# Kernel optimization log

Measured on AMD Instinct MI355X. Metric: run time of the kernel, lower is better.

The kernel has to match this reference:

```python
import jax, jax.numpy as jnp
import numpy as np

B, N, K = 8, 2048, 16
C_IN, C_MID, C_OUT = 64, 16, 64
WH = [32, 32]
FH = [256]


def _mlp_params(key, dims, scale_keyed=True):
    ps = []
    for i in range(len(dims) - 1):
        key, k1 = jax.random.split(key)
        w = jax.random.normal(k1, (dims[i], dims[i + 1]), jnp.float32) / np.sqrt(dims[i])
        b = jnp.zeros((dims[i + 1],), jnp.float32)
        ps += [w, b]
    return ps


def setup_inputs() -> dict:
    key = jax.random.key(0)
    k1, k2, k3, k4, k5 = jax.random.split(key, 5)
    groups = jnp.broadcast_to(jnp.arange(N, dtype=jnp.int32) // K, (B, N))
    points = jax.random.normal(k1, (B, N, 3), jnp.float32)
    feats = jax.random.normal(k2, (B, N, C_IN), jnp.float32)
    point_mask = (jax.random.uniform(k3, (B, N)) > 0.1).astype(jnp.float32)
    w1, b1, w2, b2, w3, b3 = _mlp_params(k4, [3] + WH + [C_MID])
    f1, fb1, f2, fb2 = _mlp_params(k5, [C_IN * C_MID] + FH + [C_OUT])
    return {"groups": groups, "points": points, "feats": feats,
            "point_mask": point_mask,
            "w1": w1, "b1": b1, "w2": w2, "b2": b2, "w3": w3, "b3": b3,
            "f1": f1, "fb1": fb1, "f2": f2, "fb2": fb2}


def _neighbor_idxs(groups):
    # matches[b,i,j] = groups[b,i]==groups[b,j]; torch .nonzero yields, per (b,i),
    # the matching j in increasing order -> stable argsort of ~matches, take first K.
    matches = groups[:, :, None] == groups[:, None, :]            # [B,N,N]
    return jnp.argsort((~matches).astype(jnp.int32), axis=-1)[:, :, :K]  # [B,N,K]


def reference(groups, points, feats, point_mask,
              w1, b1, w2, b2, w3, b3, f1, fb1, f2, fb2):
    idxs = _neighbor_idxs(groups)                                  # [B,N,K] int
    gather = jax.vmap(lambda arr, ix: arr[ix])                     # per-batch gather
    nb_pts = gather(points, idxs)                                  # [B,N,K,3]
    nb_feats = gather(feats, idxs)                                 # [B,N,K,C_IN]
    rel = points[:, :, None, :] - nb_pts                           # [B,N,K,3] (xy encoding = identity)

    # weight_conv: pointwise MLP 3 -> 32 -> 32 -> C_MID, then explicit ReLU
    h = jax.nn.relu(rel @ w1 + b1)
    h = jax.nn.relu(h @ w2 + b2)
    m = jax.nn.relu(h @ w3 + b3)                                   # [B,N,K,C_MID]

    tmask = gather(point_mask, idxs)                               # [B,N,K]
    m = m * tmask[..., None]
    nb_feats = nb_feats * tmask[..., None]

    # per-(point) matmul: [C_MID,K] x [K,C_IN] -> flatten C_MID-major
    e = jnp.einsum('bnkm,bnkc->bnmc', m, nb_feats)                 # [B,N,C_MID,C_IN]
    e = e.reshape(B, N, C_MID * C_IN)

    # final_conv: pointwise MLP 1024 -> 256 -> C_OUT
    h2 = jax.nn.relu(e @ f1 + fb1)
    out = h2 @ f2 + fb2                                            # [B,N,C_OUT]
    return out
```

## Files before the change

kernel.cpp:

```cpp
#include <hip/hip_runtime.h>

typedef unsigned short u16;
typedef short bf16x8 __attribute__((ext_vector_type(8)));
typedef float f32x4  __attribute__((ext_vector_type(4)));
typedef u16   u16x4  __attribute__((ext_vector_type(4)));

__device__ __forceinline__ u16 f2bf(float f) {
  union { float f; unsigned int i; } v; v.f = f;
  unsigned int r = (v.i + 0x7FFFu + ((v.i >> 16) & 1u)) >> 16;
  return (u16)r;
}

__global__ __launch_bounds__(256) void repack_k(const float* __restrict__ f1,
                                                const float* __restrict__ f2,
                                                u16* __restrict__ f1p,
                                                u16* __restrict__ f2p) {
  const int o = blockIdx.x * 256 + threadIdx.x;
  if (o < 262144) {
    const int j = o & 7, n = (o >> 3) & 255, kb = o >> 11;
    f1p[o] = f2bf(f1[(kb * 8 + j) * 256 + n]);
  }
  if (o < 16384) {
    const int j = o & 7, n = (o >> 3) & 63, kb = o >> 9;
    f2p[o] = f2bf(f2[(kb * 8 + j) * 64 + n]);
  }
}

__global__ __launch_bounds__(256, 4) void mlp_einsum_k(
    const float* __restrict__ points, const float* __restrict__ feats,
    const float* __restrict__ pmask,
    const float* __restrict__ w1, const float* __restrict__ b1,
    const float* __restrict__ w2, const float* __restrict__ b2,
    const float* __restrict__ w3, const float* __restrict__ b3,
    const float* __restrict__ f1, const float* __restrict__ f2,
    u16* __restrict__ f1p, u16* __restrict__ f2p,
    u16* __restrict__ Eg) {
  const int gi = blockIdx.x;
  const int bb = blockIdx.y;
  const int base = gi * 16;
  const int t = threadIdx.x;

  __shared__ float Pl[16][3];
  __shared__ float Mask[16];
  __shared__ float F[1024];
  __shared__ float Ml[16 * 16 * 20];

  {
    const int o = (bb * 128 + gi) * 256 + t;
    { const int j = o & 7, n = (o >> 3) & 255, kb = o >> 11;
      f1p[o] = f2bf(f1[(kb * 8 + j) * 256 + n]); }
    if (o < 16384) {
      const int j = o & 7, n = (o >> 3) & 63, kb = o >> 9;
      f2p[o] = f2bf(f2[(kb * 8 + j) * 64 + n]);
    }
  }

  if (t < 16) {
    Mask[t] = pmask[bb * 2048 + base + t];
    const int p = (bb * 2048 + base + t) * 3;
    Pl[t][0] = points[p + 0];
    Pl[t][1] = points[p + 1];
    Pl[t][2] = points[p + 2];
  }
  __syncthreads();

  {
    const int k = t >> 4;
    const float mk = Mask[k];
    const f32x4 fv =
        *(const f32x4*)&feats[(size_t)(bb * 2048 + base) * 64 + t * 4];
    f32x4 fs = { fv.x * mk, fv.y * mk, fv.z * mk, fv.w * mk };
    *(f32x4*)&F[t * 4] = fs;
  }
  {
    const int i = t >> 4, k = t & 15;
    const float r0 = Pl[i][0] - Pl[k][0];
    const float r1 = Pl[i][1] - Pl[k][1];
    const float r2 = Pl[i][2] - Pl[k][2];
    float h1[32];
#pragma unroll
    for (int o = 0; o < 32; ++o) {
      float a = b1[o];
      a = fmaf(r0, w1[o], a);
      a = fmaf(r1, w1[32 + o], a);
      a = fmaf(r2, w1[64 + o], a);
      h1[o] = fmaxf(a, 0.f);
    }
    float h2[32];
#pragma unroll
    for (int o = 0; o < 32; ++o) h2[o] = b2[o];
#pragma unroll
    for (int j = 0; j < 32; ++j) {
      const float hj = h1[j];
      const float* w = &w2[j * 32];
#pragma unroll
      for (int o = 0; o < 32; ++o) h2[o] = fmaf(hj, w[o], h2[o]);
    }
#pragma unroll
    for (int o = 0; o < 32; ++o) h2[o] = fmaxf(h2[o], 0.f);
    float mo[16];
#pragma unroll
    for (int o = 0; o < 16; ++o) mo[o] = b3[o];
#pragma unroll
    for (int j = 0; j < 32; ++j) {
      const float hj = h2[j];
      const float* w = &w3[j * 16];
#pragma unroll
      for (int o = 0; o < 16; ++o) mo[o] = fmaf(hj, w[o], mo[o]);
    }
    const float mk = Mask[k];
    float* Mrow = &Ml[(i * 16 + k) * 20];
#pragma unroll
    for (int o = 0; o < 16; ++o) Mrow[o] = fmaxf(mo[o], 0.f) * mk;
  }
  __syncthreads();

  {
    const int i = t >> 4;
    const int c0 = (t & 15) * 4;
    float acc[16][4] = {};
#pragma unroll
    for (int k = 0; k < 16; ++k) {
      const float* Fr = &F[k * 64 + c0];
      const float f0 = Fr[0], fA = Fr[1], fB = Fr[2], fC = Fr[3];
      const float* Mrow = &Ml[(i * 16 + k) * 20];
#pragma unroll
      for (int mi = 0; mi < 16; ++mi) {
        const float mv = Mrow[mi];
        acc[mi][0] = fmaf(mv, f0, acc[mi][0]);
        acc[mi][1] = fmaf(mv, fA, acc[mi][1]);
        acc[mi][2] = fmaf(mv, fB, acc[mi][2]);
        acc[mi][3] = fmaf(mv, fC, acc[mi][3]);
      }
    }
    u16* Erow = Eg + (size_t)(bb * 2048 + base + i) * 1024;
#pragma unroll
    for (int mi = 0; mi < 16; ++mi) {
      u16x4 v = { f2bf(acc[mi][0]), f2bf(acc[mi][1]),
                  f2bf(acc[mi][2]), f2bf(acc[mi][3]) };
      *(u16x4*)&Erow[mi * 64 + c0] = v;
    }
  }
}

#define STAGE(bf_, kc_)                                                        \
  do {                                                                         \
    const int rl_ = lane >> 3;                                       \
    const int sg_ = (lane & 7) ^ rl_;         \
    const u16* s0_ =                                                           \
        Eg + (size_t)(R + wv * 8 + rl_) * 1024 + (kc_) + sg_ * 8;              \
    u16* d0_ = &Asw[bf_][(wv * 8) * 64];            \
    u16* d1_ = &Asw[bf_][(32 + wv * 8) * 64];                                  \
    __builtin_amdgcn_global_load_lds(                                          \
        (const __attribute__((address_space(1))) void*)s0_,                    \
        (__attribute__((address_space(3))) void*)d0_, 16, 0, 0);               \
    __builtin_amdgcn_global_load_lds(                                          \
        (const __attribute__((address_space(1))) void*)(s0_ + 32 * 1024),      \
        (__attribute__((address_space(3))) void*)d1_, 16, 0, 0);               \
  } while (0)

__global__ __launch_bounds__(256) void gemm_k(
    const u16* __restrict__ Eg, const u16* __restrict__ f1p,
    const float* __restrict__ fb1, const u16* __restrict__ f2p,
    const float* __restrict__ fb2, float* __restrict__ out) {
  const int R = blockIdx.x * 64;
  const int t = threadIdx.x;
  const int wv = t >> 6, lane = t & 63;
  const int q = lane >> 4, r16 = lane & 15;

  __shared__ __align__(16) u16 Asw[3][64 * 64];
  __shared__ __align__(16) u16 H2[64 * 264];

  const int nb = wv * 64;
  f32x4 acc[4][4] = {};

  STAGE(0, 0);
  STAGE(1, 64);
  int cur = 0, stg = 2;
  for (int c = 0; c < 16; ++c) {
    if (c < 15) asm volatile("s_waitcnt vmcnt(2)" ::: "memory");
    else        asm volatile("s_waitcnt vmcnt(0)" ::: "memory");
    __builtin_amdgcn_s_barrier();

    bf16x8 bv[2][4];
#pragma unroll
    for (int ksl = 0; ksl < 2; ++ksl) {
      const int kb = c * 8 + ksl * 4 + q;
#pragma unroll
      for (int nt = 0; nt < 4; ++nt)
        bv[ksl][nt] =
            *(const bf16x8*)&f1p[(size_t)(kb * 256 + nb + nt * 16 + r16) * 8];
    }
    bf16x8 a[2][4];
#pragma unroll
    for (int ksl = 0; ksl < 2; ++ksl)
#pragma unroll
      for (int rt = 0; rt < 4; ++rt) {
        const int r = rt * 16 + r16;
        const int g = (ksl * 4 + q) ^ (r & 7);
        a[ksl][rt] = *(const bf16x8*)&Asw[cur][r * 64 + g * 8];
      }
    __builtin_amdgcn_sched_barrier(0);
    if (c <= 13) STAGE(stg, (c + 2) * 64);
    __builtin_amdgcn_sched_barrier(0);
#pragma unroll
    for (int ksl = 0; ksl < 2; ++ksl)
#pragma unroll
      for (int nt = 0; nt < 4; ++nt)
#pragma unroll
        for (int rt = 0; rt < 4; ++rt)
          acc[rt][nt] = __builtin_amdgcn_mfma_f32_16x16x32_bf16(
              a[ksl][rt], bv[ksl][nt], acc[rt][nt], 0, 0, 0);
    cur = (cur == 2) ? 0 : cur + 1;
    stg = (stg == 2) ? 0 : stg + 1;
  }

#pragma unroll
  for (int nt = 0; nt < 4; ++nt) {
    const int col = nb + nt * 16 + r16;
    const float bias = fb1[col];
#pragma unroll
    for (int rt = 0; rt < 4; ++rt)
#pragma unroll
      for (int r = 0; r < 4; ++r)
        H2[(rt * 16 + q * 4 + r) * 264 + col] =
            f2bf(fmaxf(acc[rt][nt][r] + bias, 0.f));
  }
  __syncthreads();

  const int n0 = wv * 16;
  const float bias2 = fb2[n0 + r16];
#pragma unroll
  for (int rt = 0; rt < 4; ++rt) {
    f32x4 a2 = {};
#pragma unroll
    for (int ks = 0; ks < 8; ++ks) {
      const bf16x8 av =
          *(const bf16x8*)&H2[(rt * 16 + r16) * 264 + ks * 32 + q * 8];
      const bf16x8 b2v =
          *(const bf16x8*)&f2p[(size_t)((ks * 4 + q) * 64 + n0 + r16) * 8];
      a2 = __builtin_amdgcn_mfma_f32_16x16x32_bf16(av, b2v, a2, 0, 0, 0);
    }
#pragma unroll
    for (int r = 0; r < 4; ++r)
      out[(size_t)(R + rt * 16 + q * 4 + r) * 64 + n0 + r16] = a2[r] + bias2;
  }
}
#undef STAGE

__global__ __launch_bounds__(256) void fused_k(
    const float* __restrict__ points, const float* __restrict__ feats,
    const float* __restrict__ pmask,
    const float* __restrict__ w1, const float* __restrict__ b1,
    const float* __restrict__ w2, const float* __restrict__ b2,
    const float* __restrict__ w3, const float* __restrict__ b3,
    const u16* __restrict__ f1p, const float* __restrict__ fb1,
    const u16* __restrict__ f2p, const float* __restrict__ fb2,
    float* __restrict__ out) {
  const int gi = blockIdx.x;
  const int bb = blockIdx.y;
  const int base = gi * 16;
  const int t = threadIdx.x;

  __shared__ float Wl[1712];
  __shared__ float Pl[16][3];
  __shared__ float Mask[16];
  __shared__ float F[1024];
  __shared__ __align__(16) u16 E[16 * 1032];
  __shared__ __align__(16) union {
    float Ml[16 * 16 * 17];
    u16   H2[16 * 264];
  } U;

  for (int idx = t; idx < 96;   idx += 256) Wl[idx]        = w1[idx];
  for (int idx = t; idx < 32;   idx += 256) Wl[96 + idx]   = b1[idx];
  for (int idx = t; idx < 1024; idx += 256) Wl[128 + idx]  = w2[idx];
  for (int idx = t; idx < 32;   idx += 256) Wl[1152 + idx] = b2[idx];
  for (int idx = t; idx < 512;  idx += 256) Wl[1184 + idx] = w3[idx];
  for (int idx = t; idx < 16;   idx += 256) Wl[1696 + idx] = b3[idx];
  if (t < 16) {
    Mask[t] = pmask[bb * 2048 + base + t];
    const int p = (bb * 2048 + base + t) * 3;
    Pl[t][0] = points[p + 0];
    Pl[t][1] = points[p + 1];
    Pl[t][2] = points[p + 2];
  }
  __syncthreads();

  for (int e = t; e < 1024; e += 256) {
    const int k = e >> 6;
    F[e] = feats[(bb * 2048 + base) * 64 + e] * Mask[k];
  }
  {
    const int i = t >> 4, k = t & 15;
    const float r0 = Pl[i][0] - Pl[k][0];
    const float r1 = Pl[i][1] - Pl[k][1];
    const float r2 = Pl[i][2] - Pl[k][2];
    float h1[32];
#pragma unroll
    for (int o = 0; o < 32; ++o) {
      float a = Wl[96 + o];
      a = fmaf(r0, Wl[o], a);
      a = fmaf(r1, Wl[32 + o], a);
      a = fmaf(r2, Wl[64 + o], a);
      h1[o] = fmaxf(a, 0.f);
    }
    float h2[32];
#pragma unroll
    for (int o = 0; o < 32; ++o) h2[o] = Wl[1152 + o];
#pragma unroll
    for (int j = 0; j < 32; ++j) {
      const float hj = h1[j];
      const float* w = &Wl[128 + j * 32];
#pragma unroll
      for (int o = 0; o < 32; ++o) h2[o] = fmaf(hj, w[o], h2[o]);
    }
#pragma unroll
    for (int o = 0; o < 32; ++o) h2[o] = fmaxf(h2[o], 0.f);
    float mo[16];
#pragma unroll
    for (int o = 0; o < 16; ++o) mo[o] = Wl[1696 + o];
#pragma unroll
    for (int j = 0; j < 32; ++j) {
      const float hj = h2[j];
      const float* w = &Wl[1184 + j * 16];
#pragma unroll
      for (int o = 0; o < 16; ++o) mo[o] = fmaf(hj, w[o], mo[o]);
    }
    const float mk = Mask[k];
    float* Mrow = &U.Ml[(i * 16 + k) * 17];
#pragma unroll
    for (int o = 0; o < 16; ++o) Mrow[o] = fmaxf(mo[o], 0.f) * mk;
  }
  __syncthreads();

  {
    const int i = t >> 4;
    const int c0 = (t & 15) * 4;
    float acc[16][4] = {};
#pragma unroll
    for (int k = 0; k < 16; ++k) {
      const float* Fr = &F[k * 64 + c0];
      const float f0 = Fr[0], fA = Fr[1], fB = Fr[2], fC = Fr[3];
      const float* Mrow = &U.Ml[(i * 16 + k) * 17];
#pragma unroll
      for (int mi = 0; mi < 16; ++mi) {
        const float mv = Mrow[mi];
        acc[mi][0] = fmaf(mv, f0, acc[mi][0]);
        acc[mi][1] = fmaf(mv, fA, acc[mi][1]);
        acc[mi][2] = fmaf(mv, fB, acc[mi][2]);
        acc[mi][3] = fmaf(mv, fC, acc[mi][3]);
      }
    }
    __syncthreads();
#pragma unroll
    for (int mi = 0; mi < 16; ++mi) {
      u16x4 v = { f2bf(acc[mi][0]), f2bf(acc[mi][1]), f2bf(acc[mi][2]), f2bf(acc[mi][3]) };
      *(u16x4*)&E[i * 1032 + mi * 64 + c0] = v;
    }
  }
  __syncthreads();

  {
    const int wv = t >> 6;
    const int lane = t & 63;
    const int q = lane >> 4, r16 = lane & 15;
    const int nb = wv * 64;
    f32x4 acc[4] = {};
    for (int ks = 0; ks < 32; ++ks) {
      const int k0 = ks * 32;
      const bf16x8 a = *(const bf16x8*)&E[r16 * 1032 + k0 + q * 8];
      const int kb = (k0 >> 3) + q;
#pragma unroll
      for (int nt = 0; nt < 4; ++nt) {
        const bf16x8 bvv = *(const bf16x8*)&f1p[(kb * 256 + nb + nt * 16 + r16) * 8];
        acc[nt] = __builtin_amdgcn_mfma_f32_16x16x32_bf16(a, bvv, acc[nt], 0, 0, 0);
      }
    }
    __syncthreads();
#pragma unroll
    for (int nt = 0; nt < 4; ++nt) {
      const int col = nb + nt * 16 + r16;
      const float bias = fb1[col];
#pragma unroll
      for (int r = 0; r < 4; ++r)
        U.H2[(q * 4 + r) * 264 + col] = f2bf(fmaxf(acc[nt][r] + bias, 0.f));
    }
  }
  __syncthreads();

  {
    const int wv = t >> 6;
    const int lane = t & 63;
    const int q = lane >> 4, r16 = lane & 15;
    const int n0 = wv * 16;
    f32x4 acc = {};
#pragma unroll
    for (int ks = 0; ks < 8; ++ks) {
      const int k0 = ks * 32;
      const bf16x8 a = *(const bf16x8*)&U.H2[r16 * 264 + k0 + q * 8];
      const bf16x8 bvv = *(const bf16x8*)&f2p[(((k0 >> 3) + q) * 64 + n0 + r16) * 8];
      acc = __builtin_amdgcn_mfma_f32_16x16x32_bf16(a, bvv, acc, 0, 0, 0);
    }
    const int col = n0 + r16;
    const float bias = fb2[col];
#pragma unroll
    for (int r = 0; r < 4; ++r) {
      const int row = q * 4 + r;
      out[((size_t)(bb * 2048 + base + row)) * 64 + col] = acc[r] + bias;
    }
  }
}

extern "C" void kernel_launch(void* const* d_in, const int* in_sizes, int n_in,
                              void* d_out, int out_size, void* d_ws, size_t ws_size,
                              hipStream_t stream) {
  const float* points = (const float*)d_in[1];
  const float* feats  = (const float*)d_in[2];
  const float* pmask  = (const float*)d_in[3];
  const float* w1 = (const float*)d_in[4];
  const float* b1 = (const float*)d_in[5];
  const float* w2 = (const float*)d_in[6];
  const float* b2 = (const float*)d_in[7];
  const float* w3 = (const float*)d_in[8];
  const float* b3 = (const float*)d_in[9];
  const float* f1 = (const float*)d_in[10];
  const float* fb1 = (const float*)d_in[11];
  const float* f2 = (const float*)d_in[12];
  const float* fb2 = (const float*)d_in[13];
  float* out = (float*)d_out;

  u16* f1p = (u16*)d_ws;
  u16* f2p = f1p + 262144;
  const size_t NEED = 524288 + 32768 + (size_t)16384 * 1024 * 2;

  if (ws_size >= NEED) {
    u16* Eg = f2p + 16384;
    mlp_einsum_k<<<dim3(128, 8), dim3(256), 0, stream>>>(
        points, feats, pmask, w1, b1, w2, b2, w3, b3, f1, f2, f1p, f2p, Eg);
    gemm_k<<<dim3(256), dim3(256), 0, stream>>>(Eg, f1p, fb1, f2p, fb2, out);
  } else {
    repack_k<<<dim3(1024), dim3(256), 0, stream>>>(f1, f2, f1p, f2p);
    fused_k<<<dim3(128, 8), dim3(256), 0, stream>>>(points, feats, pmask,
                                                    w1, b1, w2, b2, w3, b3,
                                                    f1p, fb1, f2p, fb2, out);
  }
}
```

Before: 130.0 us.

## Fuse weight MLP, einsum and final MLP into one 64-row mega kernel

Adds a single kernel with about 150KB of dynamic LDS. Each block computes the E matrix for 64 rows (four groups of 16) in shared memory, then runs both bf16 MFMA GEMMs directly from LDS. This removes the 32MB global round trip of the E intermediate between the two-kernel path. It also moves the f1/f2 bf16 repack back into a separate launch. The trade-off is one block per CU with only 256 blocks, so latency hiding is limited and the four group phases run serially within each block.

```diff
diff --git a/kernel.cpp b/kernel.cpp
--- a/kernel.cpp
+++ b/kernel.cpp
@@ -26,14 +26,187 @@
   }
 }
 
+#define MEGA_LDS 153088
+
+__global__ __launch_bounds__(256, 1) void mega_k(
+    const float* __restrict__ points, const float* __restrict__ feats,
+    const float* __restrict__ pmask,
+    const float* __restrict__ w1, const float* __restrict__ b1,
+    const float* __restrict__ w2, const float* __restrict__ b2,
+    const float* __restrict__ w3, const float* __restrict__ b3,
+    const u16* __restrict__ f1p, const float* __restrict__ fb1,
+    const u16* __restrict__ f2p, const float* __restrict__ fb2,
+    float* __restrict__ out) {
+  extern __shared__ __align__(16) char smem[];
+  u16*   E    = (u16*)smem;
+  u16*   H2   = (u16*)smem;
+  float* Ml   = (float*)(smem + 132096);
+  float* F    = (float*)(smem + 148736);
+  float* Pl   = (float*)(smem + 152832);
+  float* Mask = (float*)(smem + 153024);
+
+  const int t = threadIdx.x;
+  const int wv = t >> 6, lane = t & 63;
+  const int q = lane >> 4, r16 = lane & 15;
+  const int RB = blockIdx.x * 64;
+  const int bb = RB >> 11;
+  const int rowb = bb * 2048;
+
+  for (int g = 0; g < 4; ++g) {
+    const int base = (RB & 2047) + g * 16;
+    if (t < 16) {
+      Mask[t] = pmask[rowb + base + t];
+      const int p = (rowb + base + t) * 3;
+      Pl[t * 3 + 0] = points[p + 0];
+      Pl[t * 3 + 1] = points[p + 1];
+      Pl[t * 3 + 2] = points[p + 2];
+    }
+    __syncthreads();
+
+    {
+      const int k = t >> 4;
+      const float mk = Mask[k];
+      const f32x4 fv =
+          *(const f32x4*)&feats[(size_t)(rowb + base) * 64 + t * 4];
+      f32x4 fs = { fv.x * mk, fv.y * mk, fv.z * mk, fv.w * mk };
+      *(f32x4*)&F[t * 4] = fs;
+    }
+    {
+      const int i = t >> 4, k = t & 15;
+      const float r0 = Pl[i * 3 + 0] - Pl[k * 3 + 0];
+      const float r1 = Pl[i * 3 + 1] - Pl[k * 3 + 1];
+      const float r2 = Pl[i * 3 + 2] - Pl[k * 3 + 2];
+      float h1[32];
+#pragma unroll
+      for (int o = 0; o < 32; ++o) {
+        float a = b1[o];
+        a = fmaf(r0, w1[o], a);
+        a = fmaf(r1, w1[32 + o], a);
+        a = fmaf(r2, w1[64 + o], a);
+        h1[o] = fmaxf(a, 0.f);
+      }
+      float h2[32];
+#pragma unroll
+      for (int o = 0; o < 32; ++o) h2[o] = b2[o];
+#pragma unroll
+      for (int j = 0; j < 32; ++j) {
+        const float hj = h1[j];
+        const float* w = &w2[j * 32];
+#pragma unroll
+        for (int o = 0; o < 32; ++o) h2[o] = fmaf(hj, w[o], h2[o]);
+      }
+#pragma unroll
+      for (int o = 0; o < 32; ++o) h2[o] = fmaxf(h2[o], 0.f);
+      float mo[16];
+#pragma unroll
+      for (int o = 0; o < 16; ++o) mo[o] = b3[o];
+#pragma unroll
+      for (int j = 0; j < 32; ++j) {
+        const float hj = h2[j];
+        const float* w = &w3[j * 16];
+#pragma unroll
+        for (int o = 0; o < 16; ++o) mo[o] = fmaf(hj, w[o], mo[o]);
+      }
+      const float mk = Mask[k];
+      float* Mrow = &Ml[i * 260 + k * 16];
+#pragma unroll
+      for (int o = 0; o < 16; ++o) Mrow[o] = fmaxf(mo[o], 0.f) * mk;
+    }
+    __syncthreads();
+
+    {
+      const int i = t >> 4;
+      const int c0 = (t & 15) * 4;
+      float acc[16][4] = {};
+#pragma unroll
+      for (int k = 0; k < 16; ++k) {
+        const float* Fr = &F[k * 64 + c0];
+        const float f0 = Fr[0], fA = Fr[1], fB = Fr[2], fC = Fr[3];
+        const float* Mv = &Ml[i * 260 + k * 16];
+#pragma unroll
+        for (int mi = 0; mi < 16; ++mi) {
+          const float mv = Mv[mi];
+          acc[mi][0] = fmaf(mv, f0, acc[mi][0]);
+          acc[mi][1] = fmaf(mv, fA, acc[mi][1]);
+          acc[mi][2] = fmaf(mv, fB, acc[mi][2]);
+          acc[mi][3] = fmaf(mv, fC, acc[mi][3]);
+        }
+      }
+      u16* Erow = &E[(g * 16 + i) * 1032];
+#pragma unroll
+      for (int mi = 0; mi < 16; ++mi) {
+        u16x4 v = { f2bf(acc[mi][0]), f2bf(acc[mi][1]),
+                    f2bf(acc[mi][2]), f2bf(acc[mi][3]) };
+        *(u16x4*)&Erow[mi * 64 + c0] = v;
+      }
+    }
+    __syncthreads();
+  }
+
+  const int nb = wv * 64;
+  f32x4 acc[4][4] = {};
+  for (int c = 0; c < 16; ++c) {
+#pragma unroll
+    for (int ksl = 0; ksl < 2; ++ksl) {
+      const int kb = c * 8 + ksl * 4 + q;
+      bf16x8 bvv[4];
+#pragma unroll
+      for (int nt = 0; nt < 4; ++nt)
+        bvv[nt] =
+            *(const bf16x8*)&f1p[(size_t)(kb * 256 + nb + nt * 16 + r16) * 8];
+      bf16x8 av[4];
+#pragma unroll
+      for (int rt = 0; rt < 4; ++rt)
+        av[rt] = *(const bf16x8*)&E[(rt * 16 + r16) * 1032 + c * 64 +
+                                    ksl * 32 + q * 8];
+#pragma unroll
+      for (int nt = 0; nt < 4; ++nt)
+#pragma unroll
+        for (int rt = 0; rt < 4; ++rt)
+          acc[rt][nt] = __builtin_amdgcn_mfma_f32_16x16x32_bf16(
+              av[rt], bvv[nt], acc[rt][nt], 0, 0, 0);
+    }
+  }
+  __syncthreads();
+
+#pragma unroll
+  for (int nt = 0; nt < 4; ++nt) {
+    const int col = nb + nt * 16 + r16;
+    const float bias = fb1[col];
+#pragma unroll
+    for (int rt = 0; rt < 4; ++rt)
+#pragma unroll
+      for (int r = 0; r < 4; ++r)
+        H2[(rt * 16 + q * 4 + r) * 264 + col] =
+            f2bf(fmaxf(acc[rt][nt][r] + bias, 0.f));
+  }
+  __syncthreads();
+
+  const int n0 = wv * 16;
+  const float bias2 = fb2[n0 + r16];
+#pragma unroll
+  for (int rt = 0; rt < 4; ++rt) {
+    f32x4 a2 = {};
+#pragma unroll
+    for (int ks = 0; ks < 8; ++ks) {
+      const bf16x8 av =
+          *(const bf16x8*)&H2[(rt * 16 + r16) * 264 + ks * 32 + q * 8];
+      const bf16x8 b2v =
+          *(const bf16x8*)&f2p[(size_t)((ks * 4 + q) * 64 + n0 + r16) * 8];
+      a2 = __builtin_amdgcn_mfma_f32_16x16x32_bf16(av, b2v, a2, 0, 0, 0);
+    }
+#pragma unroll
+    for (int r = 0; r < 4; ++r)
+      out[(size_t)(RB + rt * 16 + q * 4 + r) * 64 + n0 + r16] = a2[r] + bias2;
+  }
+}
+
 __global__ __launch_bounds__(256, 4) void mlp_einsum_k(
     const float* __restrict__ points, const float* __restrict__ feats,
     const float* __restrict__ pmask,
     const float* __restrict__ w1, const float* __restrict__ b1,
     const float* __restrict__ w2, const float* __restrict__ b2,
     const float* __restrict__ w3, const float* __restrict__ b3,
-    const float* __restrict__ f1, const float* __restrict__ f2,
-    u16* __restrict__ f1p, u16* __restrict__ f2p,
     u16* __restrict__ Eg) {
   const int gi = blockIdx.x;
   const int bb = blockIdx.y;
@@ -43,17 +216,7 @@
   __shared__ float Pl[16][3];
   __shared__ float Mask[16];
   __shared__ float F[1024];
-  __shared__ float Ml[16 * 16 * 20];
-
-  {
-    const int o = (bb * 128 + gi) * 256 + t;
-    { const int j = o & 7, n = (o >> 3) & 255, kb = o >> 11;
-      f1p[o] = f2bf(f1[(kb * 8 + j) * 256 + n]); }
-    if (o < 16384) {
-      const int j = o & 7, n = (o >> 3) & 63, kb = o >> 9;
-      f2p[o] = f2bf(f2[(kb * 8 + j) * 64 + n]);
-    }
-  }
+  __shared__ float Ml[16 * 260];
 
   if (t < 16) {
     Mask[t] = pmask[bb * 2048 + base + t];
@@ -63,7 +226,6 @@
     Pl[t][2] = points[p + 2];
   }
   __syncthreads();
-
   {
     const int k = t >> 4;
     const float mk = Mask[k];
@@ -109,12 +271,11 @@
       for (int o = 0; o < 16; ++o) mo[o] = fmaf(hj, w[o], mo[o]);
     }
     const float mk = Mask[k];
-    float* Mrow = &Ml[(i * 16 + k) * 20];
+    float* Mrow = &Ml[i * 260 + k * 16];
 #pragma unroll
     for (int o = 0; o < 16; ++o) Mrow[o] = fmaxf(mo[o], 0.f) * mk;
   }
   __syncthreads();
-
   {
     const int i = t >> 4;
     const int c0 = (t & 15) * 4;
@@ -123,10 +284,10 @@
     for (int k = 0; k < 16; ++k) {
       const float* Fr = &F[k * 64 + c0];
       const float f0 = Fr[0], fA = Fr[1], fB = Fr[2], fC = Fr[3];
-      const float* Mrow = &Ml[(i * 16 + k) * 20];
+      const float* Mv = &Ml[i * 260 + k * 16];
 #pragma unroll
       for (int mi = 0; mi < 16; ++mi) {
-        const float mv = Mrow[mi];
+        const float mv = Mv[mi];
         acc[mi][0] = fmaf(mv, f0, acc[mi][0]);
         acc[mi][1] = fmaf(mv, fA, acc[mi][1]);
         acc[mi][2] = fmaf(mv, fB, acc[mi][2]);
@@ -145,11 +306,11 @@
 
 #define STAGE(bf_, kc_)                                                        \
   do {                                                                         \
-    const int rl_ = lane >> 3;                                       \
-    const int sg_ = (lane & 7) ^ rl_;         \
+    const int rl_ = lane >> 3;                                                 \
+    const int sg_ = (lane & 7) ^ rl_;                                          \
     const u16* s0_ =                                                           \
         Eg + (size_t)(R + wv * 8 + rl_) * 1024 + (kc_) + sg_ * 8;              \
-    u16* d0_ = &Asw[bf_][(wv * 8) * 64];            \
+    u16* d0_ = &Asw[bf_][(wv * 8) * 64];                                       \
     u16* d1_ = &Asw[bf_][(32 + wv * 8) * 64];                                  \
     __builtin_amdgcn_global_load_lds(                                          \
         (const __attribute__((address_space(1))) void*)s0_,                    \
@@ -247,170 +408,6 @@
   }
 }
 #undef STAGE
-
-__global__ __launch_bounds__(256) void fused_k(
-    const float* __restrict__ points, const float* __restrict__ feats,
-    const float* __restrict__ pmask,
-    const float* __restrict__ w1, const float* __restrict__ b1,
-    const float* __restrict__ w2, const float* __restrict__ b2,
-    const float* __restrict__ w3, const float* __restrict__ b3,
-    const u16* __restrict__ f1p, const float* __restrict__ fb1,
-    const u16* __restrict__ f2p, const float* __restrict__ fb2,
-    float* __restrict__ out) {
-  const int gi = blockIdx.x;
-  const int bb = blockIdx.y;
-  const int base = gi * 16;
-  const int t = threadIdx.x;
-
-  __shared__ float Wl[1712];
-  __shared__ float Pl[16][3];
-  __shared__ float Mask[16];
-  __shared__ float F[1024];
-  __shared__ __align__(16) u16 E[16 * 1032];
-  __shared__ __align__(16) union {
-    float Ml[16 * 16 * 17];
-    u16   H2[16 * 264];
-  } U;
-
-  for (int idx = t; idx < 96;   idx += 256) Wl[idx]        = w1[idx];
-  for (int idx = t; idx < 32;   idx += 256) Wl[96 + idx]   = b1[idx];
-  for (int idx = t; idx < 1024; idx += 256) Wl[128 + idx]  = w2[idx];
-  for (int idx = t; idx < 32;   idx += 256) Wl[1152 + idx] = b2[idx];
-  for (int idx = t; idx < 512;  idx += 256) Wl[1184 + idx] = w3[idx];
-  for (int idx = t; idx < 16;   idx += 256) Wl[1696 + idx] = b3[idx];
-  if (t < 16) {
-    Mask[t] = pmask[bb * 2048 + base + t];
-    const int p = (bb * 2048 + base + t) * 3;
-    Pl[t][0] = points[p + 0];
-    Pl[t][1] = points[p + 1];
-    Pl[t][2] = points[p + 2];
-  }
-  __syncthreads();
-
-  for (int e = t; e < 1024; e += 256) {
-    const int k = e >> 6;
-    F[e] = feats[(bb * 2048 + base) * 64 + e] * Mask[k];
-  }
-  {
-    const int i = t >> 4, k = t & 15;
-    const float r0 = Pl[i][0] - Pl[k][0];
-    const float r1 = Pl[i][1] - Pl[k][1];
-    const float r2 = Pl[i][2] - Pl[k][2];
-    float h1[32];
-#pragma unroll
-    for (int o = 0; o < 32; ++o) {
-      float a = Wl[96 + o];
-      a = fmaf(r0, Wl[o], a);
-      a = fmaf(r1, Wl[32 + o], a);
-      a = fmaf(r2, Wl[64 + o], a);
-      h1[o] = fmaxf(a, 0.f);
-    }
-    float h2[32];
-#pragma unroll
-    for (int o = 0; o < 32; ++o) h2[o] = Wl[1152 + o];
-#pragma unroll
-    for (int j = 0; j < 32; ++j) {
-      const float hj = h1[j];
-      const float* w = &Wl[128 + j * 32];
-#pragma unroll
-      for (int o = 0; o < 32; ++o) h2[o] = fmaf(hj, w[o], h2[o]);
-    }
-#pragma unroll
-    for (int o = 0; o < 32; ++o) h2[o] = fmaxf(h2[o], 0.f);
-    float mo[16];
-#pragma unroll
-    for (int o = 0; o < 16; ++o) mo[o] = Wl[1696 + o];
-#pragma unroll
-    for (int j = 0; j < 32; ++j) {
-      const float hj = h2[j];
-      const float* w = &Wl[1184 + j * 16];
-#pragma unroll
-      for (int o = 0; o < 16; ++o) mo[o] = fmaf(hj, w[o], mo[o]);
-    }
-    const float mk = Mask[k];
-    float* Mrow = &U.Ml[(i * 16 + k) * 17];
-#pragma unroll
-    for (int o = 0; o < 16; ++o) Mrow[o] = fmaxf(mo[o], 0.f) * mk;
-  }
-  __syncthreads();
-
-  {
-    const int i = t >> 4;
-    const int c0 = (t & 15) * 4;
-    float acc[16][4] = {};
-#pragma unroll
-    for (int k = 0; k < 16; ++k) {
-      const float* Fr = &F[k * 64 + c0];
-      const float f0 = Fr[0], fA = Fr[1], fB = Fr[2], fC = Fr[3];
-      const float* Mrow = &U.Ml[(i * 16 + k) * 17];
-#pragma unroll
-      for (int mi = 0; mi < 16; ++mi) {
-        const float mv = Mrow[mi];
-        acc[mi][0] = fmaf(mv, f0, acc[mi][0]);
-        acc[mi][1] = fmaf(mv, fA, acc[mi][1]);
-        acc[mi][2] = fmaf(mv, fB, acc[mi][2]);
-        acc[mi][3] = fmaf(mv, fC, acc[mi][3]);
-      }
-    }
-    __syncthreads();
-#pragma unroll
-    for (int mi = 0; mi < 16; ++mi) {
-      u16x4 v = { f2bf(acc[mi][0]), f2bf(acc[mi][1]), f2bf(acc[mi][2]), f2bf(acc[mi][3]) };
-      *(u16x4*)&E[i * 1032 + mi * 64 + c0] = v;
-    }
-  }
-  __syncthreads();
-
-  {
-    const int wv = t >> 6;
-    const int lane = t & 63;
-    const int q = lane >> 4, r16 = lane & 15;
-    const int nb = wv * 64;
-    f32x4 acc[4] = {};
-    for (int ks = 0; ks < 32; ++ks) {
-      const int k0 = ks * 32;
-      const bf16x8 a = *(const bf16x8*)&E[r16 * 1032 + k0 + q * 8];
-      const int kb = (k0 >> 3) + q;
-#pragma unroll
-      for (int nt = 0; nt < 4; ++nt) {
-        const bf16x8 bvv = *(const bf16x8*)&f1p[(kb * 256 + nb + nt * 16 + r16) * 8];
-        acc[nt] = __builtin_amdgcn_mfma_f32_16x16x32_bf16(a, bvv, acc[nt], 0, 0, 0);
-      }
-    }
-    __syncthreads();
-#pragma unroll
-    for (int nt = 0; nt < 4; ++nt) {
-      const int col = nb + nt * 16 + r16;
-      const float bias = fb1[col];
-#pragma unroll
-      for (int r = 0; r < 4; ++r)
-        U.H2[(q * 4 + r) * 264 + col] = f2bf(fmaxf(acc[nt][r] + bias, 0.f));
-    }
-  }
-  __syncthreads();
-
-  {
-    const int wv = t >> 6;
-    const int lane = t & 63;
-    const int q = lane >> 4, r16 = lane & 15;
-    const int n0 = wv * 16;
-    f32x4 acc = {};
-#pragma unroll
-    for (int ks = 0; ks < 8; ++ks) {
-      const int k0 = ks * 32;
-      const bf16x8 a = *(const bf16x8*)&U.H2[r16 * 264 + k0 + q * 8];
-      const bf16x8 bvv = *(const bf16x8*)&f2p[(((k0 >> 3) + q) * 64 + n0 + r16) * 8];
-      acc = __builtin_amdgcn_mfma_f32_16x16x32_bf16(a, bvv, acc, 0, 0, 0);
-    }
-    const int col = n0 + r16;
-    const float bias = fb2[col];
-#pragma unroll
-    for (int r = 0; r < 4; ++r) {
-      const int row = q * 4 + r;
-      out[((size_t)(bb * 2048 + base + row)) * 64 + col] = acc[r] + bias;
-    }
-  }
-}
 
 extern "C" void kernel_launch(void* const* d_in, const int* in_sizes, int n_in,
                               void* d_out, int out_size, void* d_ws, size_t ws_size,
@@ -432,17 +429,25 @@
 
   u16* f1p = (u16*)d_ws;
   u16* f2p = f1p + 262144;
-  const size_t NEED = 524288 + 32768 + (size_t)16384 * 1024 * 2;
-
-  if (ws_size >= NEED) {
+
+  static int mega_ok = -1;
+  if (mega_ok < 0) {
+    hipError_t e = hipFuncSetAttribute(
+        reinterpret_cast<const void*>(mega_k),
+        hipFuncAttributeMaxDynamicSharedMemorySize, MEGA_LDS);
+    mega_ok = (e == hipSuccess) ? 1 : 0;
+  }
+
+  if (mega_ok && ws_size >= 524288 + 32768) {
+    repack_k<<<dim3(1024), dim3(256), 0, stream>>>(f1, f2, f1p, f2p);
+    mega_k<<<dim3(256), dim3(256), MEGA_LDS, stream>>>(
+        points, feats, pmask, w1, b1, w2, b2, w3, b3,
+        f1p, fb1, f2p, fb2, out);
+  } else {
     u16* Eg = f2p + 16384;
+    repack_k<<<dim3(1024), dim3(256), 0, stream>>>(f1, f2, f1p, f2p);
     mlp_einsum_k<<<dim3(128, 8), dim3(256), 0, stream>>>(
-        points, feats, pmask, w1, b1, w2, b2, w3, b3, f1, f2, f1p, f2p, Eg);
+        points, feats, pmask, w1, b1, w2, b2, w3, b3, Eg);
     gemm_k<<<dim3(256), dim3(256), 0, stream>>>(Eg, f1p, fb1, f2p, fb2, out);
-  } else {
-    repack_k<<<dim3(1024), dim3(256), 0, stream>>>(f1, f2, f1p, f2p);
-    fused_k<<<dim3(128, 8), dim3(256), 0, stream>>>(points, feats, pmask,
-                                                    w1, b1, w2, b2, w3, b3,
-                                                    f1p, fb1, f2p, fb2, out);
-  }
-}
+  }
+}
```

Measured after the change: 169.8 us. 1.31x slower.

## Split GEMM work across eight waves and halve einsum accumulator registers

Applied to the files above, without the earlier changes.

The GEMM kernel now launches 512 threads per block: eight waves in a 2x4 grid, each computing 32 rows by 64 columns instead of 64x64. Each wave issues one LDS staging load per chunk instead of two, and the vmcnt wait is adjusted to match. In the einsum kernel, the 16x4 accumulator is computed in two halves of 8 to cut register pressure, and the Ml layout changes from a padded stride of 20 to a per-point stride of 260. The goal is more waves in flight on the GEMM and better occupancy in the einsum. The cost is that every wave in the GEMM reloads its f1p B fragments, so B traffic per block doubles.

```diff
diff --git a/kernel.cpp b/kernel.cpp
--- a/kernel.cpp
+++ b/kernel.cpp
@@ -43,7 +43,7 @@
   __shared__ float Pl[16][3];
   __shared__ float Mask[16];
   __shared__ float F[1024];
-  __shared__ float Ml[16 * 16 * 20];
+  __shared__ float Ml[16 * 260];
 
   {
     const int o = (bb * 128 + gi) * 256 + t;
@@ -109,7 +109,7 @@
       for (int o = 0; o < 16; ++o) mo[o] = fmaf(hj, w[o], mo[o]);
     }
     const float mk = Mask[k];
-    float* Mrow = &Ml[(i * 16 + k) * 20];
+    float* Mrow = &Ml[i * 260 + k * 16];
 #pragma unroll
     for (int o = 0; o < 16; ++o) Mrow[o] = fmaxf(mo[o], 0.f) * mk;
   }
@@ -118,67 +118,67 @@
   {
     const int i = t >> 4;
     const int c0 = (t & 15) * 4;
-    float acc[16][4] = {};
-#pragma unroll
-    for (int k = 0; k < 16; ++k) {
-      const float* Fr = &F[k * 64 + c0];
-      const float f0 = Fr[0], fA = Fr[1], fB = Fr[2], fC = Fr[3];
-      const float* Mrow = &Ml[(i * 16 + k) * 20];
-#pragma unroll
-      for (int mi = 0; mi < 16; ++mi) {
-        const float mv = Mrow[mi];
-        acc[mi][0] = fmaf(mv, f0, acc[mi][0]);
-        acc[mi][1] = fmaf(mv, fA, acc[mi][1]);
-        acc[mi][2] = fmaf(mv, fB, acc[mi][2]);
-        acc[mi][3] = fmaf(mv, fC, acc[mi][3]);
+    u16* Erow = Eg + (size_t)(bb * 2048 + base + i) * 1024;
+#pragma unroll
+    for (int half = 0; half < 2; ++half) {
+      float acc[8][4] = {};
+#pragma unroll
+      for (int k = 0; k < 16; ++k) {
+        const float* Fr = &F[k * 64 + c0];
+        const float f0 = Fr[0], fA = Fr[1], fB = Fr[2], fC = Fr[3];
+        const float* Mv = &Ml[i * 260 + k * 16 + half * 8];
+#pragma unroll
+        for (int mi = 0; mi < 8; ++mi) {
+          const float mv = Mv[mi];
+          acc[mi][0] = fmaf(mv, f0, acc[mi][0]);
+          acc[mi][1] = fmaf(mv, fA, acc[mi][1]);
+          acc[mi][2] = fmaf(mv, fB, acc[mi][2]);
+          acc[mi][3] = fmaf(mv, fC, acc[mi][3]);
+        }
       }
-    }
-    u16* Erow = Eg + (size_t)(bb * 2048 + base + i) * 1024;
-#pragma unroll
-    for (int mi = 0; mi < 16; ++mi) {
-      u16x4 v = { f2bf(acc[mi][0]), f2bf(acc[mi][1]),
-                  f2bf(acc[mi][2]), f2bf(acc[mi][3]) };
-      *(u16x4*)&Erow[mi * 64 + c0] = v;
+#pragma unroll
+      for (int mi = 0; mi < 8; ++mi) {
+        u16x4 v = { f2bf(acc[mi][0]), f2bf(acc[mi][1]),
+                    f2bf(acc[mi][2]), f2bf(acc[mi][3]) };
+        *(u16x4*)&Erow[(half * 8 + mi) * 64 + c0] = v;
+      }
     }
   }
 }
 
 #define STAGE(bf_, kc_)                                                        \
   do {                                                                         \
-    const int rl_ = lane >> 3;                                       \
+    const int rl_ = lane >> 3;              \
     const int sg_ = (lane & 7) ^ rl_;         \
     const u16* s0_ =                                                           \
         Eg + (size_t)(R + wv * 8 + rl_) * 1024 + (kc_) + sg_ * 8;              \
     u16* d0_ = &Asw[bf_][(wv * 8) * 64];            \
-    u16* d1_ = &Asw[bf_][(32 + wv * 8) * 64];                                  \
     __builtin_amdgcn_global_load_lds(                                          \
         (const __attribute__((address_space(1))) void*)s0_,                    \
         (__attribute__((address_space(3))) void*)d0_, 16, 0, 0);               \
-    __builtin_amdgcn_global_load_lds(                                          \
-        (const __attribute__((address_space(1))) void*)(s0_ + 32 * 1024),      \
-        (__attribute__((address_space(3))) void*)d1_, 16, 0, 0);               \
   } while (0)
 
-__global__ __launch_bounds__(256) void gemm_k(
+__global__ __launch_bounds__(512) void gemm_k(
     const u16* __restrict__ Eg, const u16* __restrict__ f1p,
     const float* __restrict__ fb1, const u16* __restrict__ f2p,
     const float* __restrict__ fb2, float* __restrict__ out) {
   const int R = blockIdx.x * 64;
   const int t = threadIdx.x;
   const int wv = t >> 6, lane = t & 63;
+  const int wr = wv >> 2, wc = wv & 3;
   const int q = lane >> 4, r16 = lane & 15;
 
   __shared__ __align__(16) u16 Asw[3][64 * 64];
   __shared__ __align__(16) u16 H2[64 * 264];
 
-  const int nb = wv * 64;
-  f32x4 acc[4][4] = {};
+  const int nb = wc * 64;
+  f32x4 acc[2][4] = {};
 
   STAGE(0, 0);
   STAGE(1, 64);
   int cur = 0, stg = 2;
   for (int c = 0; c < 16; ++c) {
-    if (c < 15) asm volatile("s_waitcnt vmcnt(2)" ::: "memory");
+    if (c < 15) asm volatile("s_waitcnt vmcnt(1)" ::: "memory");
     else        asm volatile("s_waitcnt vmcnt(0)" ::: "memory");
     __builtin_amdgcn_s_barrier();
 
@@ -191,14 +191,14 @@
         bv[ksl][nt] =
             *(const bf16x8*)&f1p[(size_t)(kb * 256 + nb + nt * 16 + r16) * 8];
     }
-    bf16x8 a[2][4];
+    bf16x8 a[2][2];
 #pragma unroll
     for (int ksl = 0; ksl < 2; ++ksl)
 #pragma unroll
-      for (int rt = 0; rt < 4; ++rt) {
-        const int r = rt * 16 + r16;
-        const int g = (ksl * 4 + q) ^ (r & 7);
-        a[ksl][rt] = *(const bf16x8*)&Asw[cur][r * 64 + g * 8];
+      for (int rt = 0; rt < 2; ++rt) {
+        const int row = wr * 32 + rt * 16 + r16;
+        const int g = (ksl * 4 + q) ^ (row & 7);
+        a[ksl][rt] = *(const bf16x8*)&Asw[cur][row * 64 + g * 8];
       }
     __builtin_amdgcn_sched_barrier(0);
     if (c <= 13) STAGE(stg, (c + 2) * 64);
@@ -208,7 +208,7 @@
 #pragma unroll
       for (int nt = 0; nt < 4; ++nt)
 #pragma unroll
-        for (int rt = 0; rt < 4; ++rt)
+        for (int rt = 0; rt < 2; ++rt)
           acc[rt][nt] = __builtin_amdgcn_mfma_f32_16x16x32_bf16(
               a[ksl][rt], bv[ksl][nt], acc[rt][nt], 0, 0, 0);
     cur = (cur == 2) ? 0 : cur + 1;
@@ -220,30 +220,31 @@
     const int col = nb + nt * 16 + r16;
     const float bias = fb1[col];
 #pragma unroll
-    for (int rt = 0; rt < 4; ++rt)
+    for (int rt = 0; rt < 2; ++rt)
 #pragma unroll
       for (int r = 0; r < 4; ++r)
-        H2[(rt * 16 + q * 4 + r) * 264 + col] =
+        H2[(wr * 32 + rt * 16 + q * 4 + r) * 264 + col] =
             f2bf(fmaxf(acc[rt][nt][r] + bias, 0.f));
   }
   __syncthreads();
 
-  const int n0 = wv * 16;
+  const int n0 = wc * 16;
   const float bias2 = fb2[n0 + r16];
 #pragma unroll
-  for (int rt = 0; rt < 4; ++rt) {
+  for (int rt = 0; rt < 2; ++rt) {
+    const int rowb = wr * 32 + rt * 16;
     f32x4 a2 = {};
 #pragma unroll
     for (int ks = 0; ks < 8; ++ks) {
       const bf16x8 av =
-          *(const bf16x8*)&H2[(rt * 16 + r16) * 264 + ks * 32 + q * 8];
+          *(const bf16x8*)&H2[(rowb + r16) * 264 + ks * 32 + q * 8];
       const bf16x8 b2v =
           *(const bf16x8*)&f2p[(size_t)((ks * 4 + q) * 64 + n0 + r16) * 8];
       a2 = __builtin_amdgcn_mfma_f32_16x16x32_bf16(av, b2v, a2, 0, 0, 0);
     }
 #pragma unroll
     for (int r = 0; r < 4; ++r)
-      out[(size_t)(R + rt * 16 + q * 4 + r) * 64 + n0 + r16] = a2[r] + bias2;
+      out[(size_t)(R + rowb + q * 4 + r) * 64 + n0 + r16] = a2[r] + bias2;
   }
 }
 #undef STAGE
@@ -438,7 +439,7 @@
     u16* Eg = f2p + 16384;
     mlp_einsum_k<<<dim3(128, 8), dim3(256), 0, stream>>>(
         points, feats, pmask, w1, b1, w2, b2, w3, b3, f1, f2, f1p, f2p, Eg);
-    gemm_k<<<dim3(256), dim3(256), 0, stream>>>(Eg, f1p, fb1, f2p, fb2, out);
+    gemm_k<<<dim3(256), dim3(512), 0, stream>>>(Eg, f1p, fb1, f2p, fb2, out);
   } else {
     repack_k<<<dim3(1024), dim3(256), 0, stream>>>(f1, f2, f1p, f2p);
     fused_k<<<dim3(128, 8), dim3(256), 0, stream>>>(points, feats, pmask,
```

Result: no change. 132.6 us (+2.0%).
